# Optimization experiments

Measured on AMD Instinct MI355X. Metric: run time of the kernel, lower is better.

The kernel has to match this reference:

```python
import jax, jax.numpy as jnp
import numpy as np

EPS = 1e-5
NEG = -9e15

def layer_norm(x, gamma, beta):
    mu = jnp.mean(x, axis=-1, keepdims=True)
    var = jnp.var(x, axis=-1, keepdims=True)
    return (x - mu) * jax.lax.rsqrt(var + EPS) * gamma + beta

def setup_inputs() -> dict:
    key = jax.random.key(0)
    ks = jax.random.split(key, 8)
    B, S, D, F = 4, 4096, 128, 512
    q = jax.random.normal(ks[0], (B, S, D), dtype=jnp.float32)
    k = jax.random.normal(ks[1], (B, S, D), dtype=jnp.float32)
    v = jax.random.normal(ks[2], (B, S, D), dtype=jnp.float32)
    w1 = jax.random.normal(ks[3], (D, F), dtype=jnp.float32) / np.sqrt(D)
    b1 = jnp.zeros((F,), dtype=jnp.float32)
    w2 = jax.random.normal(ks[4], (F, D), dtype=jnp.float32) / np.sqrt(F)
    b2 = jnp.zeros((D,), dtype=jnp.float32)
    g1 = jnp.ones((D,), dtype=jnp.float32)
    be1 = jnp.zeros((D,), dtype=jnp.float32)
    g2 = jnp.ones((D,), dtype=jnp.float32)
    be2 = jnp.zeros((D,), dtype=jnp.float32)
    return {"q": q, "k": k, "v": v, "w1": w1, "b1": b1, "w2": w2, "b2": b2,
            "g1": g1, "be1": be1, "g2": g2, "be2": be2}

def reference(q, k, v, w1, b1, w2, b2, g1, be1, g2, be2):
    d_k = q.shape[-1]
    # naive attention: [B,S,S] logits materialized, as in the original
    logits = jnp.einsum('bqd,bkd->bqk', q, k) / jnp.sqrt(jnp.asarray(d_k, q.dtype))
    attn = jax.nn.softmax(logits, axis=-1)
    attn_out = jnp.einsum('bqk,bkd->bqd', attn, v)
    x = layer_norm(attn_out, g1, be1)
    ffn = jnp.maximum(x @ w1 + b1, 0) @ w2 + b2
    return layer_norm(x + ffn, g2, be2)
```

## Files before the change

### kernel.cpp

```cpp
#include <hip/hip_runtime.h>
#include <hip/hip_bf16.h>

typedef __attribute__((ext_vector_type(8))) __bf16 bf16x8;
typedef __attribute__((ext_vector_type(4))) __bf16 bf16x4;
typedef __attribute__((ext_vector_type(4))) float f32x4;
typedef __attribute__((ext_vector_type(16))) float f32x16;

#define MFMA16(a, b, c) __builtin_amdgcn_mfma_f32_16x16x32_bf16((a), (b), (c), 0, 0, 0)
#define MFMA32(a, b, c) __builtin_amdgcn_mfma_f32_32x32x16_bf16((a), (b), (c), 0, 0, 0)

static constexpr int S_LEN = 4096;
static constexpr int DH = 128;
static constexpr int NR = 4 * S_LEN;
static constexpr float QSCALE = 0.12752551286084110f;

__device__ inline bf16x8 pack8(float4 a, float4 b) {
  bf16x8 r;
  r[0] = (__bf16)a.x; r[1] = (__bf16)a.y; r[2] = (__bf16)a.z; r[3] = (__bf16)a.w;
  r[4] = (__bf16)b.x; r[5] = (__bf16)b.y; r[6] = (__bf16)b.z; r[7] = (__bf16)b.w;
  return r;
}

__device__ __forceinline__ float fexp2(float x) {
#if __has_builtin(__builtin_amdgcn_exp2f)
  return __builtin_amdgcn_exp2f(x);
#else
  return exp2f(x);
#endif
}

__device__ __forceinline__ unsigned packbf(float a, float b) {
  union { __bf16 h[2]; unsigned u; } t;
  t.h[0] = (__bf16)a;
  t.h[1] = (__bf16)b;
  return t.u;
}

typedef __attribute__((address_space(1))) const unsigned GU32;
typedef __attribute__((address_space(3))) unsigned LU32;
__device__ __forceinline__ void gl16(const void* g, void* s) {
  __builtin_amdgcn_global_load_lds((GU32*)g, (LU32*)s, 16, 0, 0);
}

__global__ __launch_bounds__(256) void prep_all(
    const float* __restrict__ K, const float* __restrict__ V,
    const float* __restrict__ w1, const float* __restrict__ w2,
    __bf16* __restrict__ Kb, __bf16* __restrict__ VTb,
    __bf16* __restrict__ w1t, __bf16* __restrict__ w2t) {
  __shared__ float tile[32][33];
  const int bid = blockIdx.x;
  const int t = threadIdx.x;
  if (bid < 1024) {
    size_t i = ((size_t)bid * 256 + t) * 8;
    float4 a = *(const float4*)(K + i), b = *(const float4*)(K + i + 4);
    *(bf16x8*)(Kb + i) = pack8(a, b);
  } else if (bid < 3072) {
    const int bid2 = bid - 1024;
    const int b = bid2 >> 9, rem = bid2 & 511;
    const int s0 = (rem >> 2) * 32, d0 = (rem & 3) * 32;
    {
      int r = t >> 3, q = t & 7;
      float4 f = *(const float4*)(V + ((size_t)(b * S_LEN + s0 + r)) * DH + d0 + q * 4);
      tile[r][q * 4 + 0] = f.x; tile[r][q * 4 + 1] = f.y;
      tile[r][q * 4 + 2] = f.z; tile[r][q * 4 + 3] = f.w;
    }
    __syncthreads();
    {
      int dr = t >> 3, c2 = t & 7;
      bf16x4 u;
#pragma unroll
      for (int j = 0; j < 4; ++j) u[j] = (__bf16)tile[c2 * 4 + j][dr];
      int c2s = (c2 & 4) | ((c2 & 1) << 1) | ((c2 >> 1) & 1);
      *(bf16x4*)(VTb + ((size_t)(b * DH + d0 + dr)) * S_LEN + s0 + c2s * 4) = u;
    }
  } else {
    int i = (bid - 3072) * 256 + t;
    {
      int n = i >> 7, kk = i & 127;
      w1t[i] = (__bf16)w1[kk * 512 + n];
    }
    {
      int n = i >> 9, kk = i & 511;
      w2t[i] = (__bf16)w2[kk * 128 + n];
    }
  }
}

template <int NSP>
__global__ __launch_bounds__(256, 2) void attn_fa(
    const float* __restrict__ Q, const __bf16* __restrict__ Kb,
    const __bf16* __restrict__ VTb, __bf16* __restrict__ Op,
    float* __restrict__ lbuf) {
  constexpr int NTT = (S_LEN / NSP) / 64;
  __shared__ __attribute__((aligned(16))) __bf16 kl[2][64 * 128];
  __shared__ __attribute__((aligned(16))) __bf16 vt[2][128 * 64];

  const int tid = threadIdx.x;
  const int w = tid >> 6, l = tid & 63;
  const int q5 = l & 31, hi = l >> 5;
  const int bid = blockIdx.x;
  const int split = bid % NSP;
  const int qt = (bid / NSP) % 32;
  const int b = bid / (NSP * 32);
  const int R = b * S_LEN + qt * 128 + w * 32 + q5;
  const int kv0 = split * (S_LEN / NSP);

  bf16x8 qf[8];
  {
    const float* qp = Q + (size_t)R * DH + hi * 8;
#pragma unroll
    for (int kc = 0; kc < 8; ++kc) {
      float4 f0 = *(const float4*)(qp + kc * 16);
      float4 f1 = *(const float4*)(qp + kc * 16 + 4);
      f0.x *= QSCALE; f0.y *= QSCALE; f0.z *= QSCALE; f0.w *= QSCALE;
      f1.x *= QSCALE; f1.y *= QSCALE; f1.z *= QSCALE; f1.w *= QSCALE;
      qf[kc] = pack8(f0, f1);
    }
  }

  f32x16 o[4];
#pragma unroll
  for (int db = 0; db < 4; ++db) o[db] = f32x16{};
  float lsum = 0.f;

  const __bf16* kbase = Kb + (size_t)b * S_LEN * DH;
  const __bf16* vbase = VTb + (size_t)b * DH * S_LEN;

#define STAGE(BUF, S_OFF)                                                      \
  {                                                                            \
    _Pragma("unroll") for (int i = 0; i < 4; ++i) {                            \
      int r = w * 16 + i * 4 + (l >> 4);                                       \
      gl16(kbase + (size_t)((S_OFF) + r) * DH + (((l & 15) * 8) ^ ((r & 7) << 3)), \
           &kl[BUF][(w * 16 + i * 4) * 128]);                                  \
    }                                                                          \
    _Pragma("unroll") for (int i = 0; i < 4; ++i) {                            \
      int d = w * 32 + i * 8 + (l >> 3);                                       \
      gl16(vbase + (size_t)d * S_LEN + (S_OFF) + (((l & 7) * 8) ^ ((d & 7) << 3)), \
           &vt[BUF][(w * 32 + i * 8) * 64]);                                   \
    }                                                                          \
  }

  STAGE(0, kv0);
  __syncthreads();

  const int swz = (q5 & 7) << 3;

  int cur = 0;
  for (int t = 0; t < NTT; ++t) {
    if (t + 1 < NTT) STAGE(cur ^ 1, kv0 + (t + 1) * 64);

    bf16x8 pb[4];
#pragma unroll
    for (int kvb = 0; kvb < 2; ++kvb) {
      f32x16 acc = f32x16{};
      const int row = kvb * 32 + q5;
#pragma unroll
      for (int kc = 0; kc < 8; ++kc) {
        bf16x8 kf = *(const bf16x8*)&kl[cur][(row * 128 + kc * 16 + hi * 8) ^ swz];
        acc = MFMA32(kf, qf[kc], acc);
      }
      unsigned pk[4][2];
#pragma unroll
      for (int t4 = 0; t4 < 4; ++t4) {
        float e0 = fexp2(acc[4 * t4 + 0]), e1 = fexp2(acc[4 * t4 + 1]);
        float e2 = fexp2(acc[4 * t4 + 2]), e3 = fexp2(acc[4 * t4 + 3]);
        lsum += (e0 + e1) + (e2 + e3);
        pk[t4][0] = packbf(e0, e1);
        pk[t4][1] = packbf(e2, e3);
      }
#pragma unroll
      for (int kc2 = 0; kc2 < 2; ++kc2) {
        union { unsigned u[4]; bf16x8 v; } uu;
        uu.u[0] = pk[2 * kc2][0];
        uu.u[1] = pk[2 * kc2][1];
        uu.u[2] = pk[2 * kc2 + 1][0];
        uu.u[3] = pk[2 * kc2 + 1][1];
        pb[kvb * 2 + kc2] = uu.v;
      }
    }

#pragma unroll
    for (int db = 0; db < 4; ++db) {
      const int row = db * 32 + q5;
#pragma unroll
      for (int kc = 0; kc < 4; ++kc) {
        bf16x8 vf = *(const bf16x8*)&vt[cur][(row * 64 + kc * 16 + hi * 8) ^ swz];
        o[db] = MFMA32(vf, pb[kc], o[db]);
      }
    }

    __syncthreads();
    cur ^= 1;
  }
#undef STAGE

  lsum += __shfl_xor(lsum, 32);
  const float inv = 1.f / lsum;
  __bf16* orow = Op + ((size_t)split * NR + R) * DH;
#pragma unroll
  for (int db = 0; db < 4; ++db)
#pragma unroll
    for (int t4 = 0; t4 < 4; ++t4) {
      bf16x4 pk;
#pragma unroll
      for (int qi = 0; qi < 4; ++qi) pk[qi] = (__bf16)(o[db][4 * t4 + qi] * inv);
      *(bf16x4*)(orow + db * 32 + t4 * 8 + hi * 4) = pk;
    }
  if (hi == 0) lbuf[(size_t)split * NR + R] = lsum;
}

template <int NSP>
__global__ __launch_bounds__(256) void ffn_fused(
    const __bf16* __restrict__ Op, const float* __restrict__ lbuf,
    const float* __restrict__ g1, const float* __restrict__ be1,
    const __bf16* __restrict__ w1t, const __bf16* __restrict__ w2t,
    const float* __restrict__ b1, const float* __restrict__ b2,
    const float* __restrict__ g2, const float* __restrict__ be2,
    float* __restrict__ Out) {
  __shared__ __attribute__((aligned(16))) __bf16 xl[16 * 128];
  __shared__ float xr[16][132];
  __shared__ __attribute__((aligned(16))) __bf16 hl[16 * 512];
  __shared__ float part[4][16][2];

  const int tid = threadIdx.x;
  const int w = tid >> 6, l = tid & 63, lg = l >> 4, lc = l & 15;
  const int row0 = blockIdx.x * 16;

  {
    const int prow = tid >> 4, pc8 = tid & 15;
    const int R = row0 + prow;
    float v[8] = {0.f, 0.f, 0.f, 0.f, 0.f, 0.f, 0.f, 0.f};
    float den = 0.f;
#pragma unroll
    for (int s = 0; s < NSP; ++s) {
      float ls = lbuf[(size_t)s * NR + R];
      den += ls;
      bf16x8 p = *(const bf16x8*)(Op + ((size_t)s * NR + R) * DH + pc8 * 8);
#pragma unroll
      for (int j = 0; j < 8; ++j) v[j] += ls * (float)p[j];
    }
    float inv = 1.f / den;
    float sm = 0.f, sq = 0.f;
#pragma unroll
    for (int j = 0; j < 8; ++j) {
      v[j] *= inv;
      sm += v[j];
      sq += v[j] * v[j];
    }
#pragma unroll
    for (int d = 1; d < 16; d <<= 1) {
      sm += __shfl_xor(sm, d);
      sq += __shfl_xor(sq, d);
    }
    float mu = sm * (1.f / 128.f);
    float var = sq * (1.f / 128.f) - mu * mu;
    float rs = rsqrtf(var + 1e-5f);
    float4 ga = *(const float4*)(g1 + pc8 * 8), gb = *(const float4*)(g1 + pc8 * 8 + 4);
    float4 ba = *(const float4*)(be1 + pc8 * 8), bb = *(const float4*)(be1 + pc8 * 8 + 4);
    float gv[8] = {ga.x, ga.y, ga.z, ga.w, gb.x, gb.y, gb.z, gb.w};
    float bv[8] = {ba.x, ba.y, ba.z, ba.w, bb.x, bb.y, bb.z, bb.w};
    bf16x8 xb;
    float xo[8];
#pragma unroll
    for (int j = 0; j < 8; ++j) {
      xo[j] = (v[j] - mu) * rs * gv[j] + bv[j];
      xb[j] = (__bf16)xo[j];
    }
    *(bf16x8*)&xl[(prow * 128 + pc8 * 8) ^ ((prow & 7) << 3)] = xb;
    *(float4*)&xr[prow][pc8 * 8] = make_float4(xo[0], xo[1], xo[2], xo[3]);
    *(float4*)&xr[prow][pc8 * 8 + 4] = make_float4(xo[4], xo[5], xo[6], xo[7]);
  }
  __syncthreads();

  bf16x8 xf[4];
  const int m = lc;
#pragma unroll
  for (int kc = 0; kc < 4; ++kc)
    xf[kc] = *(const bf16x8*)&xl[(m * 128 + kc * 32 + lg * 8) ^ ((m & 7) << 3)];

#pragma unroll
  for (int nb = 0; nb < 8; ++nb) {
    int n0 = w * 128 + nb * 16 + lc;
    const __bf16* wp = w1t + (size_t)n0 * 128 + lg * 8;
    f32x4 acc = (f32x4){0.f, 0.f, 0.f, 0.f};
#pragma unroll
    for (int kc = 0; kc < 4; ++kc)
      acc = MFMA16(xf[kc], *(const bf16x8*)(wp + kc * 32), acc);
    float bias = b1[n0];
#pragma unroll
    for (int r = 0; r < 4; ++r) {
      int rr = lg * 4 + r;
      hl[rr * 512 + (n0 ^ (lg << 4))] = (__bf16)fmaxf(acc[r] + bias, 0.f);
    }
  }
  __syncthreads();

  const int col0 = w * 32 + lc;
  f32x4 oo[2];
#pragma unroll
  for (int nb2 = 0; nb2 < 2; ++nb2) {
    int d0 = col0 + nb2 * 16;
    const __bf16* wp2 = w2t + (size_t)d0 * 512 + lg * 8;
    f32x4 acc = (f32x4){0.f, 0.f, 0.f, 0.f};
#pragma unroll
    for (int kc = 0; kc < 16; ++kc) {
      bf16x8 ha = *(const bf16x8*)&hl[lc * 512 + ((kc * 32 + lg * 8) ^ ((lc >> 2) << 4))];
      acc = MFMA16(ha, *(const bf16x8*)(wp2 + kc * 32), acc);
    }
    oo[nb2] = acc;
  }

  float b2v[2] = {b2[col0], b2[col0 + 16]};
  float g2v[2] = {g2[col0], g2[col0 + 16]};
  float be2v[2] = {be2[col0], be2[col0 + 16]};
  float sum[4] = {0.f, 0.f, 0.f, 0.f}, sq[4] = {0.f, 0.f, 0.f, 0.f};
#pragma unroll
  for (int nb2 = 0; nb2 < 2; ++nb2)
#pragma unroll
    for (int r = 0; r < 4; ++r) {
      int rr = lg * 4 + r;
      float xv = xr[rr][col0 + nb2 * 16];
      float tv = oo[nb2][r] + b2v[nb2] + xv;
      oo[nb2][r] = tv;
      sum[r] += tv;
      sq[r] += tv * tv;
    }
#pragma unroll
  for (int r = 0; r < 4; ++r) {
#pragma unroll
    for (int d = 1; d < 16; d <<= 1) {
      sum[r] += __shfl_xor(sum[r], d);
      sq[r] += __shfl_xor(sq[r], d);
    }
    if (lc == 0) {
      part[w][lg * 4 + r][0] = sum[r];
      part[w][lg * 4 + r][1] = sq[r];
    }
  }
  __syncthreads();

#pragma unroll
  for (int r = 0; r < 4; ++r) {
    int rr = lg * 4 + r;
    float S = 0.f, Qq = 0.f;
#pragma unroll
    for (int ww = 0; ww < 4; ++ww) {
      S += part[ww][rr][0];
      Qq += part[ww][rr][1];
    }
    float mu = S * (1.f / 128.f);
    float var = Qq * (1.f / 128.f) - mu * mu;
    float rs = rsqrtf(var + 1e-5f);
#pragma unroll
    for (int nb2 = 0; nb2 < 2; ++nb2)
      Out[(size_t)(row0 + rr) * DH + col0 + nb2 * 16] =
          (oo[nb2][r] - mu) * rs * g2v[nb2] + be2v[nb2];
  }
}

extern "C" void kernel_launch(void* const* d_in, const int* in_sizes, int n_in,
                              void* d_out, int out_size, void* d_ws, size_t ws_size,
                              hipStream_t stream) {
  const float* Q = (const float*)d_in[0];
  const float* K = (const float*)d_in[1];
  const float* V = (const float*)d_in[2];
  const float* w1 = (const float*)d_in[3];
  const float* b1 = (const float*)d_in[4];
  const float* w2 = (const float*)d_in[5];
  const float* b2 = (const float*)d_in[6];
  const float* g1 = (const float*)d_in[7];
  const float* be1 = (const float*)d_in[8];
  const float* g2 = (const float*)d_in[9];
  const float* be2 = (const float*)d_in[10];
  float* Out = (float*)d_out;

  char* p = (char*)d_ws;
  __bf16* w1t = (__bf16*)p;  p += 512 * 128 * 2;
  __bf16* w2t = (__bf16*)p;  p += 128 * 512 * 2;
  __bf16* Kb  = (__bf16*)p;  p += (size_t)NR * DH * 2;
  __bf16* VTb = (__bf16*)p;  p += (size_t)NR * DH * 2;
  float* lbuf = (float*)p;   p += (size_t)4 * NR * 4;
  __bf16* Op  = (__bf16*)p;

  prep_all<<<3328, 256, 0, stream>>>(K, V, w1, w2, Kb, VTb, w1t, w2t);
  attn_fa<4><<<4 * 32 * 4, 256, 0, stream>>>(Q, Kb, VTb, Op, lbuf);
  ffn_fused<4><<<NR / 16, 256, 0, stream>>>(Op, lbuf, g1, be1, w1t, w2t, b1,
                                            b2, g2, be2, Out);
}
```

Measured before the change: 89.84 us.

## Process two query row groups per wave and raise KV split count to eight

Each wave now handles 64 query rows (two 32-row MFMA groups) instead of 32. Every K and V fragment read from shared memory feeds two MFMAs, halving LDS traffic per unit of math. To keep enough blocks in flight, the KV split factor goes from 4 to 8 when the workspace is large enough, which doubles the partial-output buffers the FFN kernel must merge. Register pressure roughly doubles for accumulators and Q fragments, which may cause spills or lower occupancy under launch_bounds(256,2).

```diff
diff --git a/kernel.cpp b/kernel.cpp
--- a/kernel.cpp
+++ b/kernel.cpp
@@ -100,28 +100,38 @@
   const int q5 = l & 31, hi = l >> 5;
   const int bid = blockIdx.x;
   const int split = bid % NSP;
-  const int qt = (bid / NSP) % 32;
-  const int b = bid / (NSP * 32);
-  const int R = b * S_LEN + qt * 128 + w * 32 + q5;
+  const int qt = (bid / NSP) % 16;
+  const int b = bid / (NSP * 16);
+  const int R0 = b * S_LEN + qt * 256 + w * 64 + q5;
+  const int R1 = R0 + 32;
   const int kv0 = split * (S_LEN / NSP);
 
-  bf16x8 qf[8];
+  bf16x8 qf0[8], qf1[8];
   {
-    const float* qp = Q + (size_t)R * DH + hi * 8;
+    const float* qp0 = Q + (size_t)R0 * DH + hi * 8;
+    const float* qp1 = Q + (size_t)R1 * DH + hi * 8;
 #pragma unroll
     for (int kc = 0; kc < 8; ++kc) {
-      float4 f0 = *(const float4*)(qp + kc * 16);
-      float4 f1 = *(const float4*)(qp + kc * 16 + 4);
+      float4 f0 = *(const float4*)(qp0 + kc * 16);
+      float4 f1 = *(const float4*)(qp0 + kc * 16 + 4);
       f0.x *= QSCALE; f0.y *= QSCALE; f0.z *= QSCALE; f0.w *= QSCALE;
       f1.x *= QSCALE; f1.y *= QSCALE; f1.z *= QSCALE; f1.w *= QSCALE;
-      qf[kc] = pack8(f0, f1);
-    }
-  }
-
-  f32x16 o[4];
-#pragma unroll
-  for (int db = 0; db < 4; ++db) o[db] = f32x16{};
-  float lsum = 0.f;
+      qf0[kc] = pack8(f0, f1);
+      float4 g0 = *(const float4*)(qp1 + kc * 16);
+      float4 g1 = *(const float4*)(qp1 + kc * 16 + 4);
+      g0.x *= QSCALE; g0.y *= QSCALE; g0.z *= QSCALE; g0.w *= QSCALE;
+      g1.x *= QSCALE; g1.y *= QSCALE; g1.z *= QSCALE; g1.w *= QSCALE;
+      qf1[kc] = pack8(g0, g1);
+    }
+  }
+
+  f32x16 o0[4], o1[4];
+#pragma unroll
+  for (int db = 0; db < 4; ++db) {
+    o0[db] = f32x16{};
+    o1[db] = f32x16{};
+  }
+  float lsum0 = 0.f, lsum1 = 0.f;
 
   const __bf16* kbase = Kb + (size_t)b * S_LEN * DH;
   const __bf16* vbase = VTb + (size_t)b * DH * S_LEN;
@@ -149,33 +159,33 @@
   for (int t = 0; t < NTT; ++t) {
     if (t + 1 < NTT) STAGE(cur ^ 1, kv0 + (t + 1) * 64);
 
-    bf16x8 pb[4];
+    union PB { unsigned u[4]; bf16x8 v; };
+    PB pb0[4], pb1[4];
 #pragma unroll
     for (int kvb = 0; kvb < 2; ++kvb) {
-      f32x16 acc = f32x16{};
+      f32x16 a0 = f32x16{}, a1 = f32x16{};
       const int row = kvb * 32 + q5;
 #pragma unroll
       for (int kc = 0; kc < 8; ++kc) {
         bf16x8 kf = *(const bf16x8*)&kl[cur][(row * 128 + kc * 16 + hi * 8) ^ swz];
-        acc = MFMA32(kf, qf[kc], acc);
-      }
-      unsigned pk[4][2];
+        a0 = MFMA32(kf, qf0[kc], a0);
+        a1 = MFMA32(kf, qf1[kc], a1);
+      }
 #pragma unroll
       for (int t4 = 0; t4 < 4; ++t4) {
-        float e0 = fexp2(acc[4 * t4 + 0]), e1 = fexp2(acc[4 * t4 + 1]);
-        float e2 = fexp2(acc[4 * t4 + 2]), e3 = fexp2(acc[4 * t4 + 3]);
-        lsum += (e0 + e1) + (e2 + e3);
-        pk[t4][0] = packbf(e0, e1);
-        pk[t4][1] = packbf(e2, e3);
-      }
-#pragma unroll
-      for (int kc2 = 0; kc2 < 2; ++kc2) {
-        union { unsigned u[4]; bf16x8 v; } uu;
-        uu.u[0] = pk[2 * kc2][0];
-        uu.u[1] = pk[2 * kc2][1];
-        uu.u[2] = pk[2 * kc2 + 1][0];
-        uu.u[3] = pk[2 * kc2 + 1][1];
-        pb[kvb * 2 + kc2] = uu.v;
+        float e0 = fexp2(a0[4 * t4 + 0]), e1 = fexp2(a0[4 * t4 + 1]);
+        float e2 = fexp2(a0[4 * t4 + 2]), e3 = fexp2(a0[4 * t4 + 3]);
+        lsum0 += (e0 + e1) + (e2 + e3);
+        pb0[kvb * 2 + (t4 >> 1)].u[(t4 & 1) * 2 + 0] = packbf(e0, e1);
+        pb0[kvb * 2 + (t4 >> 1)].u[(t4 & 1) * 2 + 1] = packbf(e2, e3);
+      }
+#pragma unroll
+      for (int t4 = 0; t4 < 4; ++t4) {
+        float e0 = fexp2(a1[4 * t4 + 0]), e1 = fexp2(a1[4 * t4 + 1]);
+        float e2 = fexp2(a1[4 * t4 + 2]), e3 = fexp2(a1[4 * t4 + 3]);
+        lsum1 += (e0 + e1) + (e2 + e3);
+        pb1[kvb * 2 + (t4 >> 1)].u[(t4 & 1) * 2 + 0] = packbf(e0, e1);
+        pb1[kvb * 2 + (t4 >> 1)].u[(t4 & 1) * 2 + 1] = packbf(e2, e3);
       }
     }
 
@@ -185,7 +195,8 @@
 #pragma unroll
       for (int kc = 0; kc < 4; ++kc) {
         bf16x8 vf = *(const bf16x8*)&vt[cur][(row * 64 + kc * 16 + hi * 8) ^ swz];
-        o[db] = MFMA32(vf, pb[kc], o[db]);
+        o0[db] = MFMA32(vf, pb0[kc].v, o0[db]);
+        o1[db] = MFMA32(vf, pb1[kc].v, o1[db]);
       }
     }
 
@@ -194,19 +205,35 @@
   }
 #undef STAGE
 
-  lsum += __shfl_xor(lsum, 32);
-  const float inv = 1.f / lsum;
-  __bf16* orow = Op + ((size_t)split * NR + R) * DH;
-#pragma unroll
-  for (int db = 0; db < 4; ++db)
-#pragma unroll
-    for (int t4 = 0; t4 < 4; ++t4) {
-      bf16x4 pk;
-#pragma unroll
-      for (int qi = 0; qi < 4; ++qi) pk[qi] = (__bf16)(o[db][4 * t4 + qi] * inv);
-      *(bf16x4*)(orow + db * 32 + t4 * 8 + hi * 4) = pk;
-    }
-  if (hi == 0) lbuf[(size_t)split * NR + R] = lsum;
+  lsum0 += __shfl_xor(lsum0, 32);
+  lsum1 += __shfl_xor(lsum1, 32);
+  const float inv0 = 1.f / lsum0, inv1 = 1.f / lsum1;
+  {
+    __bf16* orow = Op + ((size_t)split * NR + R0) * DH;
+#pragma unroll
+    for (int db = 0; db < 4; ++db)
+#pragma unroll
+      for (int t4 = 0; t4 < 4; ++t4) {
+        bf16x4 pk;
+#pragma unroll
+        for (int qi = 0; qi < 4; ++qi) pk[qi] = (__bf16)(o0[db][4 * t4 + qi] * inv0);
+        *(bf16x4*)(orow + db * 32 + t4 * 8 + hi * 4) = pk;
+      }
+    if (hi == 0) lbuf[(size_t)split * NR + R0] = lsum0;
+  }
+  {
+    __bf16* orow = Op + ((size_t)split * NR + R1) * DH;
+#pragma unroll
+    for (int db = 0; db < 4; ++db)
+#pragma unroll
+      for (int t4 = 0; t4 < 4; ++t4) {
+        bf16x4 pk;
+#pragma unroll
+        for (int qi = 0; qi < 4; ++qi) pk[qi] = (__bf16)(o1[db][4 * t4 + qi] * inv1);
+        *(bf16x4*)(orow + db * 32 + t4 * 8 + hi * 4) = pk;
+      }
+    if (hi == 0) lbuf[(size_t)split * NR + R1] = lsum1;
+  }
 }
 
 template <int NSP>
@@ -379,11 +406,21 @@
   __bf16* w2t = (__bf16*)p;  p += 128 * 512 * 2;
   __bf16* Kb  = (__bf16*)p;  p += (size_t)NR * DH * 2;
   __bf16* VTb = (__bf16*)p;  p += (size_t)NR * DH * 2;
-  float* lbuf = (float*)p;   p += (size_t)4 * NR * 4;
+  float* lbuf = (float*)p;   p += (size_t)8 * NR * 4;
   __bf16* Op  = (__bf16*)p;
 
+  const size_t base = (size_t)(p - (char*)d_ws);
+  const size_t need8 = base + (size_t)8 * NR * DH * 2;
+  const int nsp = (ws_size >= need8) ? 8 : 4;
+
   prep_all<<<3328, 256, 0, stream>>>(K, V, w1, w2, Kb, VTb, w1t, w2t);
-  attn_fa<4><<<4 * 32 * 4, 256, 0, stream>>>(Q, Kb, VTb, Op, lbuf);
-  ffn_fused<4><<<NR / 16, 256, 0, stream>>>(Op, lbuf, g1, be1, w1t, w2t, b1,
-                                            b2, g2, be2, Out);
-}
+  if (nsp == 8) {
+    attn_fa<8><<<4 * 16 * 8, 256, 0, stream>>>(Q, Kb, VTb, Op, lbuf);
+    ffn_fused<8><<<NR / 16, 256, 0, stream>>>(Op, lbuf, g1, be1, w1t, w2t, b1,
+                                              b2, g2, be2, Out);
+  } else {
+    attn_fa<4><<<4 * 16 * 4, 256, 0, stream>>>(Q, Kb, VTb, Op, lbuf);
+    ffn_fused<4><<<NR / 16, 256, 0, stream>>>(Op, lbuf, g1, be1, w1t, w2t, b1,
+                                              b2, g2, be2, Out);
+  }
+}
```

Measured after the change: 195.0 us. +117.0%, slower.
